# Kernel tuning notes

Measured on AMD Instinct MI355X. Metric: run time of the kernel, lower is better.

## Reference

```python
import jax, jax.numpy as jnp
import numpy as np

S, B, E, H = 2048, 2, 1024, 16
D = E // H


def setup_inputs() -> dict:
    key = jax.random.key(0)
    k1, k2, k3, k4 = jax.random.split(key, 4)
    x = jax.random.normal(k1, (S, B, E), dtype=jnp.float32)
    # xavier_uniform for [3E, E] and [O, E]
    lim_qkv = float(np.sqrt(6.0 / (3 * E + E)))
    lim_out = float(np.sqrt(6.0 / (E + E)))
    w_qkv = jax.random.uniform(k2, (3 * E, E), jnp.float32, -lim_qkv, lim_qkv)
    b_qkv = jnp.zeros((3 * E,), jnp.float32)
    w_out = jax.random.uniform(k3, (E, E), jnp.float32, -lim_out, lim_out)
    b_out = jnp.zeros((E,), jnp.float32)
    return {"x": x, "w_qkv": w_qkv, "b_qkv": b_qkv, "w_out": w_out, "b_out": b_out}


def reference(x, w_qkv, b_qkv, w_out, b_out):
    # x: [S, B, E] (seq-first, as in the torch module)
    s, b, e = x.shape
    scaling = jnp.asarray(np.sqrt(D), x.dtype)
    qkv = jnp.einsum('sbe,fe->sbf', x, w_qkv) + b_qkv          # [S,B,3E]
    q, k, v = jnp.split(qkv, 3, axis=-1)
    q = q.reshape(s, b, H, D)
    k = k.reshape(s, b, H, D)
    v = v.reshape(s, b, H, D)
    # scores [B,H,S,S]; note original divides by sqrt(head_dim)
    scores = jnp.einsum('sbhd,tbhd->bhst', q, k) / scaling
    attn_w = jax.nn.softmax(scores.astype(jnp.float32), axis=-1).astype(scores.dtype)
    # dropout p=0.1 is identity in eval mode (training=False)
    attn = jnp.einsum('bhst,tbhd->sbhd', attn_w, v).reshape(s, b, e)
    out = jnp.einsum('sbe,oe->sbo', attn, w_out) + b_out        # [S,B,O]
    attn_avg = attn_w.mean(axis=1)                              # [B,S,S]
    return out, attn_avg
```

## Files before the change

kernel.cpp:

```cpp
#include <hip/hip_runtime.h>

#define SEQ   2048
#define BATCH 2
#define NH    16
#define HD    64
#define EMB   1024

#define QSCALE 0.18033688011112042f

using bf16x8 = __attribute__((ext_vector_type(8))) short;
using f32x4  = __attribute__((ext_vector_type(4))) float;
using f32x16 = __attribute__((ext_vector_type(16))) float;

__device__ __forceinline__ unsigned short f2bf(float f) {
  unsigned int u = __float_as_uint(f);
  u += 0x7FFFu + ((u >> 16) & 1u);
  return (unsigned short)(u >> 16);
}
__device__ __forceinline__ unsigned pk_bf16(float lo, float hi) {
  unsigned r;
  asm("v_cvt_pk_bf16_f32 %0, %1, %2" : "=v"(r) : "v"(lo), "v"(hi));
  return r;
}
__device__ __forceinline__ void gload16(const void* g, void* l) {
  __builtin_amdgcn_global_load_lds(
      (const __attribute__((address_space(1))) unsigned int*)g,
      (__attribute__((address_space(3))) unsigned int*)l, 16, 0, 0);
}

__global__ __launch_bounds__(256) void cvt3_f32_bf16(
    const float* __restrict__ a, int na4,
    const float* __restrict__ b, int nb4,
    const float* __restrict__ c, int nc4,
    unsigned short* __restrict__ oa,
    unsigned short* __restrict__ ob,
    unsigned short* __restrict__ oc) {
  int i = blockIdx.x * 256 + threadIdx.x;
  const float* src;
  unsigned short* dst;
  int j = i;
  if (j < na4) { src = a; dst = oa; }
  else if ((j -= na4) < nb4) { src = b; dst = ob; }
  else { j -= nb4; if (j >= nc4) return; src = c; dst = oc; }
  float4 v = reinterpret_cast<const float4*>(src)[j];
  ushort4 o;
  o.x = f2bf(v.x); o.y = f2bf(v.y); o.z = f2bf(v.z); o.w = f2bf(v.w);
  reinterpret_cast<ushort4*>(dst)[j] = o;
}

template <int EPI>
__global__ __launch_bounds__(256) void gemm_bt(
    const unsigned short* __restrict__ A,
    const unsigned short* __restrict__ B,
    const float* __restrict__ bias,
    float* __restrict__ Cf,
    unsigned short* __restrict__ Qb,
    unsigned short* __restrict__ Kb,
    unsigned short* __restrict__ VTb,
    int M, int N, int K) {
  __shared__ int4 As[128][8];
  __shared__ int4 Bs[128][8];
  const int tid = threadIdx.x;
  const int wid = tid >> 6, lane = tid & 63;
  const int wm = wid >> 1, wn = wid & 1;
  const int lg = lane >> 4, lr = lane & 15;
  const int lr8 = lane >> 3;
  const int lc8 = (lane & 7) ^ lr8;
  const int nbx = gridDim.x;
  const int nwg = nbx * gridDim.y;
  const int id = blockIdx.x + nbx * blockIdx.y;
  const int swz = (id & 7) * (nwg >> 3) + (id >> 3);
  const int row0 = (swz % nbx) * 128, col0 = (swz / nbx) * 128;
  f32x4 acc[4][4] = {};
  for (int k0 = 0; k0 < K; k0 += 64) {
#pragma unroll
    for (int i = 0; i < 4; i++) {
      const int rb = wid * 32 + i * 8;
      gload16(&A[(size_t)(row0 + rb + lr8) * K + k0 + lc8 * 8], &As[rb][0]);
      gload16(&B[(size_t)(col0 + rb + lr8) * K + k0 + lc8 * 8], &Bs[rb][0]);
    }
    __syncthreads();
#pragma unroll
    for (int ks = 0; ks < 2; ks++) {
      bf16x8 af[4], bfr[4];
#pragma unroll
      for (int mi = 0; mi < 4; mi++) {
        int r = wm * 64 + mi * 16 + lr;
        af[mi] = *reinterpret_cast<const bf16x8*>(&As[r][(ks * 4 + lg) ^ (r & 7)]);
      }
#pragma unroll
      for (int ni = 0; ni < 4; ni++) {
        int r = wn * 64 + ni * 16 + lr;
        bfr[ni] = *reinterpret_cast<const bf16x8*>(&Bs[r][(ks * 4 + lg) ^ (r & 7)]);
      }
#pragma unroll
      for (int mi = 0; mi < 4; mi++)
#pragma unroll
        for (int ni = 0; ni < 4; ni++)
          acc[mi][ni] = __builtin_amdgcn_mfma_f32_16x16x32_bf16(af[mi], bfr[ni], acc[mi][ni], 0, 0, 0);
    }
    __syncthreads();
  }
#pragma unroll
  for (int mi = 0; mi < 4; mi++)
#pragma unroll
    for (int ni = 0; ni < 4; ni++) {
      const int row_b = row0 + wm * 64 + mi * 16 + lg * 4;
      const int col = col0 + wn * 64 + ni * 16 + lr;
      const float bs = bias[col];
      float v0 = acc[mi][ni][0] + bs;
      float v1 = acc[mi][ni][1] + bs;
      float v2 = acc[mi][ni][2] + bs;
      float v3 = acc[mi][ni][3] + bs;
      if (EPI == 0) {
        Cf[(size_t)(row_b + 0) * N + col] = v0;
        Cf[(size_t)(row_b + 1) * N + col] = v1;
        Cf[(size_t)(row_b + 2) * N + col] = v2;
        Cf[(size_t)(row_b + 3) * N + col] = v3;
      } else {
        const int which = col >> 10, rr = col & 1023;
        const int hh = rr >> 6, d = rr & 63;
        if (which == 2) {
          const int s0 = row_b >> 1;
          ushort2 p0; p0.x = f2bf(v0); p0.y = f2bf(v2);
          ushort2 p1; p1.x = f2bf(v1); p1.y = f2bf(v3);
          *reinterpret_cast<ushort2*>(&VTb[((size_t)((0 * NH + hh) * HD + d)) * SEQ + s0]) = p0;
          *reinterpret_cast<ushort2*>(&VTb[((size_t)((1 * NH + hh) * HD + d)) * SEQ + s0]) = p1;
        } else {
          unsigned short* dst = which == 0 ? Qb : Kb;
          const float sc = (which == 0) ? QSCALE : 1.0f;
          float vv[4] = {v0 * sc, v1 * sc, v2 * sc, v3 * sc};
#pragma unroll
          for (int r = 0; r < 4; r++) {
            int s = (row_b + r) >> 1, bb = r & 1;
            dst[(size_t)((bb * NH + hh) * SEQ + s) * HD + d] = f2bf(vv[r]);
          }
        }
      }
    }
}

__global__ __launch_bounds__(256, 2) void attn1(
    const unsigned short* __restrict__ Qb,
    const unsigned short* __restrict__ Kb,
    const unsigned short* __restrict__ VTb,
    unsigned short* __restrict__ attn_bf,
    float* __restrict__ lbuf) {
  __shared__ int4 Kt[2][64][8];
  __shared__ int4 Vt[2][64][8];
  const int tid = threadIdx.x;
  const int wid = tid >> 6, lane = tid & 63;
  const int l31 = lane & 31, lhi = lane >> 5;
  const int lr8 = lane >> 3;
  const int lc8 = (lane & 7) ^ lr8;
  const int L = blockIdx.x;
  const int v = (L & 7) * 64 + (L >> 3);
  const int bh = v >> 4, stile = v & 15;
  const int b = bh >> 4, h = bh & 15;
  const int s0 = stile * 128 + wid * 32;
  const unsigned short* Qg = Qb + (size_t)bh * SEQ * HD;
  const unsigned short* Kg = Kb + (size_t)bh * SEQ * HD;
  const unsigned short* VTg = VTb + (size_t)bh * HD * SEQ;

  bf16x8 qf[4];
#pragma unroll
  for (int ks = 0; ks < 4; ks++)
    qf[ks] = *reinterpret_cast<const bf16x8*>(Qg + (size_t)(s0 + l31) * HD + ks * 16 + lhi * 8);

  auto stage = [&](int tg, int buf) {
#pragma unroll
    for (int i = 0; i < 2; i++) {
      const int rb = wid * 16 + i * 8;
      gload16(Kg + (size_t)(tg * 64 + rb + lr8) * HD + lc8 * 8, &Kt[buf][rb][0]);
      gload16(VTg + (size_t)(rb + lr8) * SEQ + tg * 64 + lc8 * 8, &Vt[buf][rb][0]);
    }
  };

  const f32x16 fz = {};
  f32x16 o[2] = {};
  float ls = 0.f;
  bf16x8 paq[4];
  bf16x8 vfr[2][4];

  auto qk = [&](int cur, f32x16 st[2]) {
#pragma unroll
    for (int ti = 0; ti < 2; ti++) {
      const int row = ti * 32 + l31;
      bf16x8 kf = *reinterpret_cast<const bf16x8*>(&Kt[cur][row][(lhi) ^ (row & 7)]);
      st[ti] = __builtin_amdgcn_mfma_f32_32x32x16_bf16(kf, qf[0], fz, 0, 0, 0);
    }
#pragma unroll
    for (int ks = 1; ks < 4; ks++)
#pragma unroll
      for (int ti = 0; ti < 2; ti++) {
        const int row = ti * 32 + l31;
        bf16x8 kf = *reinterpret_cast<const bf16x8*>(&Kt[cur][row][(ks * 2 + lhi) ^ (row & 7)]);
        st[ti] = __builtin_amdgcn_mfma_f32_32x32x16_bf16(kf, qf[ks], st[ti], 0, 0, 0);
      }
  };
  auto softpack = [&](const f32x16 st[2]) {
    float p[32];
    float psum = 0.f;
#pragma unroll
    for (int ti = 0; ti < 2; ti++)
#pragma unroll
      for (int r = 0; r < 16; r++) {
        float e = __builtin_amdgcn_exp2f(st[ti][r]);
        p[ti * 16 + r] = e;
        psum += e;
      }
    ls += psum;
#pragma unroll
    for (int c = 0; c < 4; c++) {
      const int ti = c >> 1, cc = c & 1;
      const int pb = ti * 16 + cc * 8;
      unsigned w0 = pk_bf16(p[pb + 0], p[pb + 1]);
      unsigned w1 = pk_bf16(p[pb + 2], p[pb + 3]);
      unsigned w2 = pk_bf16(p[pb + 4], p[pb + 5]);
      unsigned w3 = pk_bf16(p[pb + 6], p[pb + 7]);
      asm volatile("v_permlane32_swap_b32 %0, %1" : "+v"(w0), "+v"(w2));
      asm volatile("v_permlane32_swap_b32 %0, %1" : "+v"(w1), "+v"(w3));
      union { unsigned u[4]; bf16x8 v; } pa;
      pa.u[0] = w0; pa.u[1] = w1; pa.u[2] = w2; pa.u[3] = w3;
      paq[c] = pa.v;
    }
  };
  auto loadv = [&](int cur) {
#pragma unroll
    for (int dt = 0; dt < 2; dt++)
#pragma unroll
      for (int c = 0; c < 4; c++) {
        const int row = dt * 32 + l31;
        vfr[dt][c] = *reinterpret_cast<const bf16x8*>(&Vt[cur][row][(c * 2 + lhi) ^ (row & 7)]);
      }
  };

  stage(0, 0);
  __syncthreads();

  {
    stage(1, 1);
    f32x16 st[2];
    __builtin_amdgcn_s_setprio(1);
    qk(0, st);
    __builtin_amdgcn_s_setprio(0);
    softpack(st);
    loadv(0);
    __syncthreads();
  }

  for (int t = 1; t < 32; t++) {
    const int cur = t & 1;
    if (t + 1 < 32) stage(t + 1, cur ^ 1);
    f32x16 st[2];
    __builtin_amdgcn_s_setprio(1);
#pragma unroll
    for (int c = 0; c < 4; c++)
#pragma unroll
      for (int dt = 0; dt < 2; dt++)
        o[dt] = __builtin_amdgcn_mfma_f32_32x32x16_bf16(paq[c], vfr[dt][c], o[dt], 0, 0, 0);
    qk(cur, st);
    __builtin_amdgcn_s_setprio(0);
    softpack(st);
    loadv(cur);
    __syncthreads();
  }
#pragma unroll
  for (int c = 0; c < 4; c++)
#pragma unroll
    for (int dt = 0; dt < 2; dt++)
      o[dt] = __builtin_amdgcn_mfma_f32_32x32x16_bf16(paq[c], vfr[dt][c], o[dt], 0, 0, 0);

  ls += __shfl_xor(ls, 32, 64);
  if (lhi == 0)
    lbuf[(size_t)bh * SEQ + s0 + l31] = ls;

#pragma unroll
  for (int r = 0; r < 16; r++) {
    const int s_off = (r & 3) + 8 * (r >> 2) + 4 * lhi;
    float denom = __shfl(ls, s_off, 64);
    float inv = __builtin_amdgcn_rcpf(denom);
    const int s = s0 + s_off;
#pragma unroll
    for (int dt = 0; dt < 2; dt++) {
      float ov = o[dt][r] * inv;
      attn_bf[((size_t)s * BATCH + b) * EMB + h * HD + dt * 32 + l31] = f2bf(ov);
    }
  }
}

__global__ __launch_bounds__(256) void attn2(
    const unsigned short* __restrict__ Qb,
    const unsigned short* __restrict__ Kb,
    const float* __restrict__ lbuf,
    float* __restrict__ avg_out) {
  const int b = blockIdx.z;
  const int s0 = blockIdx.y * 64;
  const int tc0 = blockIdx.x * 256;
  __shared__ int4 Qs[64][8];
  __shared__ int4 Ks[2][64][8];
  __shared__ float lls[NH][64];
  const int tid = threadIdx.x;
  const int wid = tid >> 6, lane = tid & 63;
  const int wm = wid >> 1, wn = wid & 1;
  const int lg = lane >> 4, lr = lane & 15;
  const int lr8 = lane >> 3;
  const int lc8 = (lane & 7) ^ lr8;

  for (int i = tid; i < NH * 64; i += 256) {
    int hh = i >> 6, r = i & 63;
    lls[hh][r] = 1.0f / ((float)NH * lbuf[(b * NH + hh) * SEQ + s0 + r]);
  }

  const size_t bh0 = (size_t)(b * NH) * SEQ;

  auto stageK = [&](const unsigned short* src, int buf) {
#pragma unroll
    for (int i = 0; i < 2; i++) {
      const int rb = wid * 16 + i * 8;
      gload16(src + (size_t)(rb + lr8) * HD + lc8 * 8, &Ks[buf][rb][0]);
    }
  };
  auto stageQ = [&](const unsigned short* src) {
#pragma unroll
    for (int i = 0; i < 2; i++) {
      const int rb = wid * 16 + i * 8;
      gload16(src + (size_t)(rb + lr8) * HD + lc8 * 8, &Qs[rb][0]);
    }
  };

  stageQ(Qb + (bh0 + s0) * HD);
  stageK(Kb + (bh0 + tc0) * HD, 0);
  __syncthreads();

  const f32x4 fz4 = {};
  f32x4 avg[4][2][2] = {};

  for (int h = 0; h < NH; h++) {
    bf16x8 af[2][2];
#pragma unroll
    for (int mi = 0; mi < 2; mi++) {
      int r = wm * 32 + mi * 16 + lr;
#pragma unroll
      for (int ks = 0; ks < 2; ks++)
        af[mi][ks] = *reinterpret_cast<const bf16x8*>(&Qs[r][(ks * 4 + lg) ^ (r & 7)]);
    }
    float linv[2][4];
#pragma unroll
    for (int mi = 0; mi < 2; mi++)
#pragma unroll
      for (int r = 0; r < 4; r++)
        linv[mi][r] = lls[h][wm * 32 + mi * 16 + lg * 4 + r];

    const unsigned short* Kgh = Kb + (bh0 + (size_t)h * SEQ + tc0) * HD;

    for (int t0 = 0; t0 < 4; t0++) {
      const int cur = t0 & 1;
      if (t0 < 3) {
        stageK(Kgh + (size_t)(t0 + 1) * 64 * HD, cur ^ 1);
      } else if (h + 1 < NH) {
        stageK(Kb + (bh0 + (size_t)(h + 1) * SEQ + tc0) * HD, cur ^ 1);
        stageQ(Qb + (bh0 + (size_t)(h + 1) * SEQ + s0) * HD);
      }
      f32x4 sacc[2][2];
      __builtin_amdgcn_s_setprio(1);
#pragma unroll
      for (int ks = 0; ks < 2; ks++) {
        bf16x8 bk[2];
#pragma unroll
        for (int ni = 0; ni < 2; ni++) {
          int rk = wn * 32 + ni * 16 + lr;
          bk[ni] = *reinterpret_cast<const bf16x8*>(&Ks[cur][rk][(ks * 4 + lg) ^ (rk & 7)]);
        }
#pragma unroll
        for (int mi = 0; mi < 2; mi++)
#pragma unroll
          for (int ni = 0; ni < 2; ni++)
            sacc[mi][ni] = __builtin_amdgcn_mfma_f32_16x16x32_bf16(
                af[mi][ks], bk[ni], ks == 0 ? fz4 : sacc[mi][ni], 0, 0, 0);
      }
      __builtin_amdgcn_s_setprio(0);
#pragma unroll
      for (int mi = 0; mi < 2; mi++)
#pragma unroll
        for (int ni = 0; ni < 2; ni++)
#pragma unroll
          for (int r = 0; r < 4; r++)
            avg[t0][mi][ni][r] += __builtin_amdgcn_exp2f(sacc[mi][ni][r]) * linv[mi][r];
      __syncthreads();
    }
  }

#pragma unroll
  for (int t0 = 0; t0 < 4; t0++)
#pragma unroll
    for (int mi = 0; mi < 2; mi++)
#pragma unroll
      for (int ni = 0; ni < 2; ni++)
#pragma unroll
        for (int r = 0; r < 4; r++) {
          int s = s0 + wm * 32 + mi * 16 + lg * 4 + r;
          int t = tc0 + t0 * 64 + wn * 32 + ni * 16 + lr;
          avg_out[((size_t)b * SEQ + s) * SEQ + t] = avg[t0][mi][ni][r];
        }
}

extern "C" void kernel_launch(void* const* d_in, const int* in_sizes, int n_in,
                              void* d_out, int out_size, void* d_ws, size_t ws_size,
                              hipStream_t stream) {
  const float* x     = (const float*)d_in[0];
  const float* w_qkv = (const float*)d_in[1];
  const float* b_qkv = (const float*)d_in[2];
  const float* w_out = (const float*)d_in[3];
  const float* b_out = (const float*)d_in[4];
  float* out = (float*)d_out;
  float* avg = out + (size_t)SEQ * BATCH * EMB;

  char* ws = (char*)d_ws;
  size_t off = 0;
  unsigned short* x_bf    = (unsigned short*)(ws + off); off += (size_t)SEQ * BATCH * EMB * 2;
  unsigned short* wqkv_bf = (unsigned short*)(ws + off); off += (size_t)3 * EMB * EMB * 2;
  unsigned short* wout_bf = (unsigned short*)(ws + off); off += (size_t)EMB * EMB * 2;
  unsigned short* Qbuf    = (unsigned short*)(ws + off); off += (size_t)BATCH * NH * SEQ * HD * 2;
  unsigned short* Kbuf    = (unsigned short*)(ws + off); off += (size_t)BATCH * NH * SEQ * HD * 2;
  unsigned short* VTbuf   = (unsigned short*)(ws + off); off += (size_t)BATCH * NH * HD * SEQ * 2;
  unsigned short* attn_bf = (unsigned short*)(ws + off); off += (size_t)SEQ * BATCH * EMB * 2;
  float*          lbuf    = (float*)(ws + off);          off += (size_t)BATCH * NH * SEQ * 4;

  {
    const int na4 = SEQ * BATCH * EMB / 4;
    const int nb4 = 3 * EMB * EMB / 4;
    const int nc4 = EMB * EMB / 4;
    const int nblk = (na4 + nb4 + nc4 + 255) / 256;
    cvt3_f32_bf16<<<nblk, 256, 0, stream>>>(x, na4, w_qkv, nb4, w_out, nc4,
                                            x_bf, wqkv_bf, wout_bf);
  }

  gemm_bt<1><<<dim3(SEQ * BATCH / 128, 3 * EMB / 128), 256, 0, stream>>>(
      x_bf, wqkv_bf, b_qkv, nullptr, Qbuf, Kbuf, VTbuf, SEQ * BATCH, 3 * EMB, EMB);

  attn1<<<512, 256, 0, stream>>>(Qbuf, Kbuf, VTbuf, attn_bf, lbuf);

  attn2<<<dim3(SEQ / 256, SEQ / 64, BATCH), 256, 0, stream>>>(Qbuf, Kbuf, lbuf, avg);

  gemm_bt<0><<<dim3(SEQ * BATCH / 128, EMB / 128), 256, 0, stream>>>(
      attn_bf, wout_bf, b_out, out, nullptr, nullptr, nullptr, SEQ * BATCH, EMB, EMB);
}
```

Baseline: 153.5 us.

## Process two heads per iteration in attn2 and drop GEMM block swizzle

The attention-average kernel now stages Q and K for two heads at once and computes both heads' score tiles between barriers. This halves the number of __syncthreads and loop iterations, at the cost of doubled LDS buffers and more live registers; launch_bounds(256,2) is added to keep occupancy. Separately, the GEMM drops its workgroup-ID swizzle in favour of direct blockIdx mapping, which may change L2 reuse.

```diff
diff --git a/kernel.cpp b/kernel.cpp
--- a/kernel.cpp
+++ b/kernel.cpp
@@ -66,11 +66,7 @@
   const int lg = lane >> 4, lr = lane & 15;
   const int lr8 = lane >> 3;
   const int lc8 = (lane & 7) ^ lr8;
-  const int nbx = gridDim.x;
-  const int nwg = nbx * gridDim.y;
-  const int id = blockIdx.x + nbx * blockIdx.y;
-  const int swz = (id & 7) * (nwg >> 3) + (id >> 3);
-  const int row0 = (swz % nbx) * 128, col0 = (swz / nbx) * 128;
+  const int row0 = blockIdx.x * 128, col0 = blockIdx.y * 128;
   f32x4 acc[4][4] = {};
   for (int k0 = 0; k0 < K; k0 += 64) {
 #pragma unroll
@@ -289,7 +285,7 @@
   }
 }
 
-__global__ __launch_bounds__(256) void attn2(
+__global__ __launch_bounds__(256, 2) void attn2(
     const unsigned short* __restrict__ Qb,
     const unsigned short* __restrict__ Kb,
     const float* __restrict__ lbuf,
@@ -297,8 +293,8 @@
   const int b = blockIdx.z;
   const int s0 = blockIdx.y * 64;
   const int tc0 = blockIdx.x * 256;
-  __shared__ int4 Qs[64][8];
-  __shared__ int4 Ks[2][64][8];
+  __shared__ int4 Qs[2][64][8];
+  __shared__ int4 Ks[2][2][64][8];
   __shared__ float lls[NH][64];
   const int tid = threadIdx.x;
   const int wid = tid >> 6, lane = tid & 63;
@@ -314,79 +310,94 @@
 
   const size_t bh0 = (size_t)(b * NH) * SEQ;
 
-  auto stageK = [&](const unsigned short* src, int buf) {
+  auto stageK = [&](const unsigned short* src, int buf, int hsel) {
 #pragma unroll
     for (int i = 0; i < 2; i++) {
       const int rb = wid * 16 + i * 8;
-      gload16(src + (size_t)(rb + lr8) * HD + lc8 * 8, &Ks[buf][rb][0]);
-    }
-  };
-  auto stageQ = [&](const unsigned short* src) {
+      gload16(src + (size_t)(rb + lr8) * HD + lc8 * 8, &Ks[buf][hsel][rb][0]);
+    }
+  };
+  auto stageQ = [&](const unsigned short* src, int hsel) {
 #pragma unroll
     for (int i = 0; i < 2; i++) {
       const int rb = wid * 16 + i * 8;
-      gload16(src + (size_t)(rb + lr8) * HD + lc8 * 8, &Qs[rb][0]);
-    }
-  };
-
-  stageQ(Qb + (bh0 + s0) * HD);
-  stageK(Kb + (bh0 + tc0) * HD, 0);
+      gload16(src + (size_t)(rb + lr8) * HD + lc8 * 8, &Qs[hsel][rb][0]);
+    }
+  };
+
+  stageQ(Qb + (bh0 + s0) * HD, 0);
+  stageQ(Qb + (bh0 + SEQ + s0) * HD, 1);
+  stageK(Kb + (bh0 + tc0) * HD, 0, 0);
+  stageK(Kb + (bh0 + SEQ + tc0) * HD, 0, 1);
   __syncthreads();
 
   const f32x4 fz4 = {};
   f32x4 avg[4][2][2] = {};
 
-  for (int h = 0; h < NH; h++) {
-    bf16x8 af[2][2];
-#pragma unroll
-    for (int mi = 0; mi < 2; mi++) {
-      int r = wm * 32 + mi * 16 + lr;
-#pragma unroll
-      for (int ks = 0; ks < 2; ks++)
-        af[mi][ks] = *reinterpret_cast<const bf16x8*>(&Qs[r][(ks * 4 + lg) ^ (r & 7)]);
-    }
-    float linv[2][4];
-#pragma unroll
-    for (int mi = 0; mi < 2; mi++)
-#pragma unroll
-      for (int r = 0; r < 4; r++)
-        linv[mi][r] = lls[h][wm * 32 + mi * 16 + lg * 4 + r];
-
-    const unsigned short* Kgh = Kb + (bh0 + (size_t)h * SEQ + tc0) * HD;
+  for (int hp = 0; hp < NH / 2; hp++) {
+    const int h0 = 2 * hp, h1 = h0 + 1;
+    bf16x8 af[2][2][2];
+#pragma unroll
+    for (int hh = 0; hh < 2; hh++)
+#pragma unroll
+      for (int mi = 0; mi < 2; mi++) {
+        int r = wm * 32 + mi * 16 + lr;
+#pragma unroll
+        for (int ks = 0; ks < 2; ks++)
+          af[hh][mi][ks] = *reinterpret_cast<const bf16x8*>(&Qs[hh][r][(ks * 4 + lg) ^ (r & 7)]);
+      }
+    float linv[2][2][4];
+#pragma unroll
+    for (int hh = 0; hh < 2; hh++)
+#pragma unroll
+      for (int mi = 0; mi < 2; mi++)
+#pragma unroll
+        for (int r = 0; r < 4; r++)
+          linv[hh][mi][r] = lls[h0 + hh][wm * 32 + mi * 16 + lg * 4 + r];
+
+    const unsigned short* Kg0 = Kb + (bh0 + (size_t)h0 * SEQ + tc0) * HD;
+    const unsigned short* Kg1 = Kb + (bh0 + (size_t)h1 * SEQ + tc0) * HD;
 
     for (int t0 = 0; t0 < 4; t0++) {
       const int cur = t0 & 1;
       if (t0 < 3) {
-        stageK(Kgh + (size_t)(t0 + 1) * 64 * HD, cur ^ 1);
-      } else if (h + 1 < NH) {
-        stageK(Kb + (bh0 + (size_t)(h + 1) * SEQ + tc0) * HD, cur ^ 1);
-        stageQ(Qb + (bh0 + (size_t)(h + 1) * SEQ + s0) * HD);
-      }
-      f32x4 sacc[2][2];
+        stageK(Kg0 + (size_t)(t0 + 1) * 64 * HD, cur ^ 1, 0);
+        stageK(Kg1 + (size_t)(t0 + 1) * 64 * HD, cur ^ 1, 1);
+      } else if (hp + 1 < NH / 2) {
+        stageK(Kb + (bh0 + (size_t)(h0 + 2) * SEQ + tc0) * HD, cur ^ 1, 0);
+        stageK(Kb + (bh0 + (size_t)(h1 + 2) * SEQ + tc0) * HD, cur ^ 1, 1);
+        stageQ(Qb + (bh0 + (size_t)(h0 + 2) * SEQ + s0) * HD, 0);
+        stageQ(Qb + (bh0 + (size_t)(h1 + 2) * SEQ + s0) * HD, 1);
+      }
+      f32x4 sacc[2][2][2];
       __builtin_amdgcn_s_setprio(1);
 #pragma unroll
-      for (int ks = 0; ks < 2; ks++) {
-        bf16x8 bk[2];
-#pragma unroll
-        for (int ni = 0; ni < 2; ni++) {
-          int rk = wn * 32 + ni * 16 + lr;
-          bk[ni] = *reinterpret_cast<const bf16x8*>(&Ks[cur][rk][(ks * 4 + lg) ^ (rk & 7)]);
+      for (int hh = 0; hh < 2; hh++)
+#pragma unroll
+        for (int ks = 0; ks < 2; ks++) {
+          bf16x8 bk[2];
+#pragma unroll
+          for (int ni = 0; ni < 2; ni++) {
+            int rk = wn * 32 + ni * 16 + lr;
+            bk[ni] = *reinterpret_cast<const bf16x8*>(&Ks[cur][hh][rk][(ks * 4 + lg) ^ (rk & 7)]);
+          }
+#pragma unroll
+          for (int mi = 0; mi < 2; mi++)
+#pragma unroll
+            for (int ni = 0; ni < 2; ni++)
+              sacc[hh][mi][ni] = __builtin_amdgcn_mfma_f32_16x16x32_bf16(
+                  af[hh][mi][ks], bk[ni], ks == 0 ? fz4 : sacc[hh][mi][ni], 0, 0, 0);
         }
+      __builtin_amdgcn_s_setprio(0);
+#pragma unroll
+      for (int hh = 0; hh < 2; hh++)
 #pragma unroll
         for (int mi = 0; mi < 2; mi++)
 #pragma unroll
           for (int ni = 0; ni < 2; ni++)
-            sacc[mi][ni] = __builtin_amdgcn_mfma_f32_16x16x32_bf16(
-                af[mi][ks], bk[ni], ks == 0 ? fz4 : sacc[mi][ni], 0, 0, 0);
-      }
-      __builtin_amdgcn_s_setprio(0);
-#pragma unroll
-      for (int mi = 0; mi < 2; mi++)
-#pragma unroll
-        for (int ni = 0; ni < 2; ni++)
-#pragma unroll
-          for (int r = 0; r < 4; r++)
-            avg[t0][mi][ni][r] += __builtin_amdgcn_exp2f(sacc[mi][ni][r]) * linv[mi][r];
+#pragma unroll
+            for (int r = 0; r < 4; r++)
+              avg[t0][mi][ni][r] += __builtin_amdgcn_exp2f(sacc[hh][mi][ni][r]) * linv[hh][mi][r];
       __syncthreads();
     }
   }
```

After: 145.1 us. 5.5% less time.
